# Kernel tuning notes

Measured on AMD Instinct MI355X. Metric: run time of the kernel, lower is better.

## Reference

```python
import jax, jax.numpy as jnp
import numpy as np

D_MODEL = 1024


def setup_inputs() -> dict:
    key = jax.random.key(0)
    ks = jax.random.split(key, 8)
    B, S, D = 32, 2048, D_MODEL
    scale = 1.0 / np.sqrt(D)
    return {
        "query": jax.random.normal(ks[0], (B, D), dtype=jnp.float32),
        "keys": jax.random.normal(ks[1], (B, S, D), dtype=jnp.float32),
        "Wq_w": jax.random.normal(ks[2], (D, D), dtype=jnp.float32) * scale,
        "Wq_b": jax.random.normal(ks[3], (D,), dtype=jnp.float32) * 0.01,
        "Wk_w": jax.random.normal(ks[4], (D, D), dtype=jnp.float32) * scale,
        "Wk_b": jax.random.normal(ks[5], (D,), dtype=jnp.float32) * 0.01,
        "v_w": jax.random.normal(ks[6], (D,), dtype=jnp.float32) * scale,
        "v_b": jax.random.normal(ks[7], (1,), dtype=jnp.float32) * 0.01,
    }


def reference(query, keys, Wq_w, Wq_b, Wk_w, Wk_b, v_w, v_b):
    # q: [B, 1, D], k: [B, S, D]
    q = (query @ Wq_w.T + Wq_b)[:, None, :]
    k = keys @ Wk_w.T + Wk_b
    # additive (Bahdanau) scores: [B, S]
    scores = jnp.einsum("bsd,d->bs", jnp.tanh(q + k), v_w) + v_b[0]
    attn = jax.nn.softmax(scores, axis=-1)
    # weighted sum over original keys: [B, D]
    context = jnp.einsum("bs,bsd->bd", attn, keys)
    return (context, attn)
```

## Files before the change

### kernel.cpp

```cpp
#include <hip/hip_runtime.h>
#include <cstddef>
#include <cstdint>

#define BATCH 32
#define SEQ 2048
#define DM 1024

typedef __attribute__((ext_vector_type(8))) _Float16 half8v;
typedef __attribute__((ext_vector_type(4))) _Float16 half4v;
typedef __attribute__((ext_vector_type(2))) __fp16 fp16x2;
typedef __attribute__((ext_vector_type(4))) float f32x4;

__device__ _Float16 g_Bpk[8 * 8 * 32 * 4 * 16 * 8];
__device__ float g_q[BATCH * DM];
__device__ float g_sp[16][BATCH * SEQ];

__device__ __forceinline__ float tanh_fast(float x) {
    float e = __expf(2.0f * x);
    return 1.0f - 2.0f / (e + 1.0f);
}

__global__ __launch_bounds__(256) void packb_kernel(const float* __restrict__ Wk_w) {
    int blk = blockIdx.x;
    int nc = blk >> 3, sub = blk & 7;
    int t = threadIdx.x;
    int row = t & 15, kgrp = (t >> 4) & 3, kt0 = t >> 6;
    const float* src = Wk_w + (size_t)(nc * 128 + sub * 16 + row) * DM;
    _Float16* dst = g_Bpk + (size_t)blk * 16384;
#pragma unroll
    for (int pass = 0; pass < 8; ++pass) {
        int kt = pass * 4 + kt0;
        float4 w0 = *reinterpret_cast<const float4*>(src + kt * 32 + kgrp * 8);
        float4 w1 = *reinterpret_cast<const float4*>(src + kt * 32 + kgrp * 8 + 4);
        union { _Float16 f[8]; half8v v; } h;
        h.f[0] = (_Float16)w0.x; h.f[1] = (_Float16)w0.y;
        h.f[2] = (_Float16)w0.z; h.f[3] = (_Float16)w0.w;
        h.f[4] = (_Float16)w1.x; h.f[5] = (_Float16)w1.y;
        h.f[6] = (_Float16)w1.z; h.f[7] = (_Float16)w1.w;
        *reinterpret_cast<half8v*>(&dst[(size_t)((kt * 4 + kgrp) * 16 + row) * 8]) = h.v;
    }
}

__global__ __launch_bounds__(256) void init_kernel(float* __restrict__ context) {
    int idx = blockIdx.x * 256 + threadIdx.x;
    if (idx < BATCH * DM) context[idx] = 0.f;
}

__global__ __launch_bounds__(256) void qproj_kernel(const float* __restrict__ query,
                                                    const float* __restrict__ Wq_w,
                                                    const float* __restrict__ Wq_b) {
    int d = blockIdx.x;
    int t = threadIdx.x;
    __shared__ float wrow[DM];
    __shared__ float part[8][32];
    reinterpret_cast<float4*>(wrow)[t] =
        reinterpret_cast<const float4*>(Wq_w + (size_t)d * DM)[t];
    __syncthreads();
    int b = t & 31, seg = t >> 5;
    const float4* qp = reinterpret_cast<const float4*>(query + b * DM + seg * 128);
    const float4* wp = reinterpret_cast<const float4*>(wrow + seg * 128);
    float acc = 0.f;
#pragma unroll
    for (int i = 0; i < 32; ++i) {
        float4 qv = qp[i];
        float4 wv = wp[i];
        acc += qv.x * wv.x + qv.y * wv.y + qv.z * wv.z + qv.w * wv.w;
    }
    part[seg][b] = acc;
    __syncthreads();
    if (t < 32) {
        float s = Wq_b[d];
#pragma unroll
        for (int g = 0; g < 8; ++g) s += part[g][t];
        g_q[t * DM + d] = s;
    }
}

#define BM 128
#define BN 128
#define NT2 16

__global__ __launch_bounds__(256, 3) void scores_kernel(const float* __restrict__ keys,
                                                        const float* __restrict__ Wk_b,
                                                        const float* __restrict__ v_w) {
    __shared__ _Float16 AhS[2][2][4][BM + 1][8];

    const unsigned bid = blockIdx.x;
    const unsigned L = (bid & 7u) * 512u + (bid >> 3);
    const int mtile = (int)(L >> 3);
    const int nchunk = (int)(L & 7u);
    const int m0 = mtile * BM;
    const int n0 = nchunk * BN;
    const int b = m0 >> 11;

    const int t = threadIdx.x;
    const int w = t >> 6, l = t & 63;
    const int wm = w >> 1, wn = w & 1;
    const int lr = l & 15, lg = l >> 4;

    const int akc = (l & 7) >> 1;
    const int aoff = ((l & 7) & 1) * 4;
    const float* Ap = keys + (size_t)(m0 + w * 32 + (l >> 3)) * DM + (l & 7) * 4;

    const _Float16* Bp = g_Bpk + ((size_t)(nchunk * 8 + wn * 4)) * 16384
                               + (size_t)(l >> 4) * 128 + (size_t)(l & 15) * 8;

    float4 as0[4], as1[4];
    half8v bE[4], bO[4];

    f32x4 acc[4][4];
#pragma unroll
    for (int mi = 0; mi < 4; ++mi)
#pragma unroll
        for (int ni = 0; ni < 4; ++ni)
#pragma unroll
            for (int c = 0; c < 4; ++c) acc[mi][ni][c] = 0.f;

#define LOAD_A2(kt)                                                              \
    {                                                                            \
        _Pragma("unroll") for (int j = 0; j < 4; ++j)                            \
            as0[j] = *reinterpret_cast<const float4*>(                           \
                Ap + (size_t)j * 8 * DM + (kt) * 64);                            \
        _Pragma("unroll") for (int j = 0; j < 4; ++j)                            \
            as1[j] = *reinterpret_cast<const float4*>(                           \
                Ap + (size_t)j * 8 * DM + (kt) * 64 + 32);                       \
    }
#define LOAD_BF(ks, dst)                                                         \
    {                                                                            \
        _Pragma("unroll") for (int ni = 0; ni < 4; ++ni)                         \
            dst[ni] = *reinterpret_cast<const half8v*>(                          \
                Bp + (size_t)ni * 16384 + (size_t)(ks) * 512);                   \
    }
#define STAGE_ONE(bufi, sub, areg)                                               \
    {                                                                            \
        _Pragma("unroll") for (int j = 0; j < 4; ++j) {                          \
            const float* fa = reinterpret_cast<const float*>(&areg[j]);          \
            union { fp16x2 h2[2]; half4v v; } u;                                 \
            u.h2[0] = __builtin_amdgcn_cvt_pkrtz(fa[0], fa[1]);                  \
            u.h2[1] = __builtin_amdgcn_cvt_pkrtz(fa[2], fa[3]);                  \
            *reinterpret_cast<half4v*>(                                          \
                &AhS[bufi][sub][akc][w * 32 + j * 8 + (l >> 3)][aoff]) = u.v;    \
        }                                                                        \
    }
#define COMPUTE_S(bufi, sub, breg)                                               \
    {                                                                            \
        __builtin_amdgcn_s_setprio(1);                                           \
        _Pragma("unroll") for (int mi = 0; mi < 4; ++mi) {                       \
            half8v ahv = *reinterpret_cast<const half8v*>(                       \
                &AhS[bufi][sub][lg][wm * 64 + mi * 16 + lr][0]);                 \
            _Pragma("unroll") for (int ni = 0; ni < 4; ++ni)                     \
                acc[mi][ni] = __builtin_amdgcn_mfma_f32_16x16x32_f16(            \
                    ahv, breg[ni], acc[mi][ni], 0, 0, 0);                        \
        }                                                                        \
        __builtin_amdgcn_s_setprio(0);                                          \
    }
#define SYNC()                                                                   \
    asm volatile("s_waitcnt lgkmcnt(0)" ::: "memory");                           \
    __builtin_amdgcn_s_barrier();                                                \
    asm volatile("" ::: "memory");

    LOAD_A2(0);
    LOAD_BF(0, bE);
    STAGE_ONE(0, 0, as0);
    STAGE_ONE(0, 1, as1);
    SYNC()

    for (int tt = 0; tt < NT2; ++tt) {
        const int cb = tt & 1;
        LOAD_BF(2 * tt + 1, bO);
        if (tt + 1 < NT2) LOAD_A2(tt + 1);
        COMPUTE_S(cb, 0, bE);
        COMPUTE_S(cb, 1, bO);
        if (tt + 1 < NT2) {
            STAGE_ONE(cb ^ 1, 0, as0);
            STAGE_ONE(cb ^ 1, 1, as1);
            LOAD_BF(2 * tt + 2, bE);
        }
        SYNC()
    }

    float qb[4], vw[4];
#pragma unroll
    for (int ni = 0; ni < 4; ++ni) {
        int n = n0 + wn * 64 + ni * 16 + lr;
        qb[ni] = g_q[b * DM + n] + Wk_b[n];
        vw[ni] = v_w[n];
    }
#pragma unroll
    for (int mi = 0; mi < 4; ++mi) {
#pragma unroll
        for (int rg = 0; rg < 4; ++rg) {
            float p = 0.f;
#pragma unroll
            for (int ni = 0; ni < 4; ++ni) {
                float val = acc[mi][ni][rg] + qb[ni];
                p += tanh_fast(val) * vw[ni];
            }
#pragma unroll
            for (int off = 8; off >= 1; off >>= 1) p += __shfl_xor(p, off, 16);
            if (lr == 0)
                g_sp[nchunk * 2 + wn][m0 + wm * 64 + mi * 16 + lg * 4 + rg] = p;
        }
    }
#undef LOAD_A2
#undef LOAD_BF
#undef STAGE_ONE
#undef COMPUTE_S
#undef SYNC
}

__global__ __launch_bounds__(256) void softmax_kernel(float* __restrict__ attn) {
    int b = blockIdx.x;
    int tid = threadIdx.x;
    __shared__ float redm[4];
    __shared__ float reds[4];
    float v[8];
    float mx = -1e30f;
#pragma unroll
    for (int i = 0; i < 8; ++i) {
        int idx = b * SEQ + i * 256 + tid;
        float s = 0.f;
#pragma unroll
        for (int pslot = 0; pslot < 16; ++pslot) s += g_sp[pslot][idx];
        v[i] = s;
        mx = fmaxf(mx, v[i]);
    }
#pragma unroll
    for (int off = 32; off >= 1; off >>= 1) mx = fmaxf(mx, __shfl_xor(mx, off));
    int wid = tid >> 6;
    if ((tid & 63) == 0) redm[wid] = mx;
    __syncthreads();
    mx = fmaxf(fmaxf(redm[0], redm[1]), fmaxf(redm[2], redm[3]));
    float sum = 0.f;
#pragma unroll
    for (int i = 0; i < 8; ++i) {
        v[i] = expf(v[i] - mx);
        sum += v[i];
    }
#pragma unroll
    for (int off = 32; off >= 1; off >>= 1) sum += __shfl_xor(sum, off);
    if ((tid & 63) == 0) reds[wid] = sum;
    __syncthreads();
    sum = reds[0] + reds[1] + reds[2] + reds[3];
    float inv = 1.f / sum;
#pragma unroll
    for (int i = 0; i < 8; ++i) attn[b * SEQ + i * 256 + tid] = v[i] * inv;
}

__global__ __launch_bounds__(256) void context_kernel(const float* __restrict__ keys,
                                                      const float* __restrict__ attn,
                                                      float* __restrict__ context) {
    int id = blockIdx.x;
    int schunk = id & 15;
    int b = id >> 4;
    int tid = threadIdx.x;
    __shared__ float a_s[128];
    if (tid < 128) a_s[tid] = attn[b * SEQ + schunk * 128 + tid];
    __syncthreads();
    const float4* kp =
        reinterpret_cast<const float4*>(keys + ((size_t)b * SEQ + schunk * 128) * DM) + tid;
    float4 acc = {0.f, 0.f, 0.f, 0.f};
#pragma unroll 4
    for (int s = 0; s < 128; ++s) {
        float4 kv = kp[(size_t)s * (DM / 4)];
        float a = a_s[s];
        acc.x += a * kv.x; acc.y += a * kv.y; acc.z += a * kv.z; acc.w += a * kv.w;
    }
    atomicAdd(&context[b * DM + tid * 4 + 0], acc.x);
    atomicAdd(&context[b * DM + tid * 4 + 1], acc.y);
    atomicAdd(&context[b * DM + tid * 4 + 2], acc.z);
    atomicAdd(&context[b * DM + tid * 4 + 3], acc.w);
}

extern "C" void kernel_launch(void* const* d_in, const int* in_sizes, int n_in,
                              void* d_out, int out_size, void* d_ws, size_t ws_size,
                              hipStream_t stream) {
    const float* query = (const float*)d_in[0];
    const float* keys  = (const float*)d_in[1];
    const float* Wq_w  = (const float*)d_in[2];
    const float* Wq_b  = (const float*)d_in[3];
    const float* Wk_w  = (const float*)d_in[4];
    const float* Wk_b  = (const float*)d_in[5];
    const float* v_w   = (const float*)d_in[6];

    float* context = (float*)d_out;
    float* attn    = context + BATCH * DM;

    hipLaunchKernelGGL(packb_kernel, dim3(64), dim3(256), 0, stream, Wk_w);
    hipLaunchKernelGGL(init_kernel, dim3(128), dim3(256), 0, stream, context);
    hipLaunchKernelGGL(qproj_kernel, dim3(DM), dim3(256), 0, stream, query, Wq_w, Wq_b);
    hipLaunchKernelGGL(scores_kernel, dim3((BATCH * SEQ / BM) * (DM / BN)), dim3(256), 0, stream,
                       keys, Wk_b, v_w);
    hipLaunchKernelGGL(softmax_kernel, dim3(BATCH), dim3(256), 0, stream, attn);
    hipLaunchKernelGGL(context_kernel, dim3(512), dim3(256), 0, stream, keys, attn, context);
}
```

Before: 255.7 us.

## Prepack keys to fp16 and stream A tiles via direct global-to-LDS loads

```diff
diff --git a/kernel.cpp b/kernel.cpp
--- a/kernel.cpp
+++ b/kernel.cpp
@@ -11,6 +11,7 @@
 typedef __attribute__((ext_vector_type(2))) __fp16 fp16x2;
 typedef __attribute__((ext_vector_type(4))) float f32x4;
 
+__device__ _Float16 g_Apk[(size_t)512 * 16 * 16 * 64 * 8];
 __device__ _Float16 g_Bpk[8 * 8 * 32 * 4 * 16 * 8];
 __device__ float g_q[BATCH * DM];
 __device__ float g_sp[16][BATCH * SEQ];
@@ -18,6 +19,33 @@
 __device__ __forceinline__ float tanh_fast(float x) {
     float e = __expf(2.0f * x);
     return 1.0f - 2.0f / (e + 1.0f);
+}
+
+__device__ __forceinline__ void gload16(const void* g, void* l) {
+    __builtin_amdgcn_global_load_lds((__attribute__((address_space(1))) void*)g,
+                                     (__attribute__((address_space(3))) void*)l, 16, 0, 0);
+}
+
+__global__ __launch_bounds__(256) void packa_kernel(const float* __restrict__ keys) {
+    int blk = blockIdx.x;
+    int mtile = blk >> 4, kt = blk & 15;
+    int t = threadIdx.x;
+    int row = t >> 1, half = t & 1;
+    int rh = row >> 6, r6 = row & 63;
+    const float* src = keys + (size_t)(mtile * 128 + row) * DM + kt * 64 + half * 32;
+    _Float16* dst = g_Apk + (size_t)blk * 8192;
+#pragma unroll
+    for (int kc = 0; kc < 4; ++kc) {
+        float4 w0 = *reinterpret_cast<const float4*>(src + kc * 8);
+        float4 w1 = *reinterpret_cast<const float4*>(src + kc * 8 + 4);
+        union { fp16x2 h2[4]; half8v v; } u;
+        u.h2[0] = __builtin_amdgcn_cvt_pkrtz(w0.x, w0.y);
+        u.h2[1] = __builtin_amdgcn_cvt_pkrtz(w0.z, w0.w);
+        u.h2[2] = __builtin_amdgcn_cvt_pkrtz(w1.x, w1.y);
+        u.h2[3] = __builtin_amdgcn_cvt_pkrtz(w1.z, w1.w);
+        int seg = (half * 4 + kc) * 2 + rh;
+        *reinterpret_cast<half8v*>(dst + (size_t)seg * 512 + r6 * 8) = u.v;
+    }
 }
 
 __global__ __launch_bounds__(256) void packb_kernel(const float* __restrict__ Wk_w) {
@@ -80,10 +108,9 @@
 #define BN 128
 #define NT2 16
 
-__global__ __launch_bounds__(256, 3) void scores_kernel(const float* __restrict__ keys,
-                                                        const float* __restrict__ Wk_b,
+__global__ __launch_bounds__(256, 4) void scores_kernel(const float* __restrict__ Wk_b,
                                                         const float* __restrict__ v_w) {
-    __shared__ _Float16 AhS[2][2][4][BM + 1][8];
+    __shared__ _Float16 AhS[2][16 * 520];
 
     const unsigned bid = blockIdx.x;
     const unsigned L = (bid & 7u) * 512u + (bid >> 3);
@@ -98,14 +125,11 @@
     const int wm = w >> 1, wn = w & 1;
     const int lr = l & 15, lg = l >> 4;
 
-    const int akc = (l & 7) >> 1;
-    const int aoff = ((l & 7) & 1) * 4;
-    const float* Ap = keys + (size_t)(m0 + w * 32 + (l >> 3)) * DM + (l & 7) * 4;
+    const int abase = (lg * 2 + wm) * 520 + lr * 8;
 
     const _Float16* Bp = g_Bpk + ((size_t)(nchunk * 8 + wn * 4)) * 16384
                                + (size_t)(l >> 4) * 128 + (size_t)(l & 15) * 8;
 
-    float4 as0[4], as1[4];
     half8v bE[4], bO[4];
 
     f32x4 acc[4][4];
@@ -116,14 +140,12 @@
 #pragma unroll
             for (int c = 0; c < 4; ++c) acc[mi][ni][c] = 0.f;
 
-#define LOAD_A2(kt)                                                              \
+#define ISSUE_A(kt, bufi)                                                        \
     {                                                                            \
-        _Pragma("unroll") for (int j = 0; j < 4; ++j)                            \
-            as0[j] = *reinterpret_cast<const float4*>(                           \
-                Ap + (size_t)j * 8 * DM + (kt) * 64);                            \
-        _Pragma("unroll") for (int j = 0; j < 4; ++j)                            \
-            as1[j] = *reinterpret_cast<const float4*>(                           \
-                Ap + (size_t)j * 8 * DM + (kt) * 64 + 32);                       \
+        const _Float16* ga = g_Apk + ((size_t)(mtile * 16 + (kt))) * 8192        \
+                           + (size_t)(w * 4) * 512 + (size_t)l * 8;              \
+        _Pragma("unroll") for (int i = 0; i < 4; ++i)                            \
+            gload16(ga + i * 512, &AhS[bufi][(w * 4 + i) * 520]);                \
     }
 #define LOAD_BF(ks, dst)                                                         \
     {                                                                            \
@@ -131,52 +153,35 @@
             dst[ni] = *reinterpret_cast<const half8v*>(                          \
                 Bp + (size_t)ni * 16384 + (size_t)(ks) * 512);                   \
     }
-#define STAGE_ONE(bufi, sub, areg)                                               \
-    {                                                                            \
-        _Pragma("unroll") for (int j = 0; j < 4; ++j) {                          \
-            const float* fa = reinterpret_cast<const float*>(&areg[j]);          \
-            union { fp16x2 h2[2]; half4v v; } u;                                 \
-            u.h2[0] = __builtin_amdgcn_cvt_pkrtz(fa[0], fa[1]);                  \
-            u.h2[1] = __builtin_amdgcn_cvt_pkrtz(fa[2], fa[3]);                  \
-            *reinterpret_cast<half4v*>(                                          \
-                &AhS[bufi][sub][akc][w * 32 + j * 8 + (l >> 3)][aoff]) = u.v;    \
-        }                                                                        \
-    }
 #define COMPUTE_S(bufi, sub, breg)                                               \
     {                                                                            \
         __builtin_amdgcn_s_setprio(1);                                           \
         _Pragma("unroll") for (int mi = 0; mi < 4; ++mi) {                       \
             half8v ahv = *reinterpret_cast<const half8v*>(                       \
-                &AhS[bufi][sub][lg][wm * 64 + mi * 16 + lr][0]);                 \
+                &AhS[bufi][abase + (sub) * 4160 + mi * 128]);                    \
             _Pragma("unroll") for (int ni = 0; ni < 4; ++ni)                     \
                 acc[mi][ni] = __builtin_amdgcn_mfma_f32_16x16x32_f16(            \
                     ahv, breg[ni], acc[mi][ni], 0, 0, 0);                        \
         }                                                                        \
         __builtin_amdgcn_s_setprio(0);                                          \
     }
-#define SYNC()                                                                   \
-    asm volatile("s_waitcnt lgkmcnt(0)" ::: "memory");                           \
-    __builtin_amdgcn_s_barrier();                                                \
+
+    ISSUE_A(0, 0);
+    LOAD_BF(0, bE);
+    asm volatile("s_waitcnt vmcnt(0)" ::: "memory");
+    __builtin_amdgcn_s_barrier();
     asm volatile("" ::: "memory");
-
-    LOAD_A2(0);
-    LOAD_BF(0, bE);
-    STAGE_ONE(0, 0, as0);
-    STAGE_ONE(0, 1, as1);
-    SYNC()
 
     for (int tt = 0; tt < NT2; ++tt) {
         const int cb = tt & 1;
+        if (tt + 1 < NT2) ISSUE_A(tt + 1, cb ^ 1);
         LOAD_BF(2 * tt + 1, bO);
-        if (tt + 1 < NT2) LOAD_A2(tt + 1);
         COMPUTE_S(cb, 0, bE);
         COMPUTE_S(cb, 1, bO);
-        if (tt + 1 < NT2) {
-            STAGE_ONE(cb ^ 1, 0, as0);
-            STAGE_ONE(cb ^ 1, 1, as1);
-            LOAD_BF(2 * tt + 2, bE);
-        }
-        SYNC()
+        if (tt + 1 < NT2) LOAD_BF(2 * tt + 2, bE);
+        asm volatile("s_waitcnt vmcnt(4)" ::: "memory");
+        __builtin_amdgcn_s_barrier();
+        asm volatile("" ::: "memory");
     }
 
     float qb[4], vw[4];
@@ -202,11 +207,9 @@
                 g_sp[nchunk * 2 + wn][m0 + wm * 64 + mi * 16 + lg * 4 + rg] = p;
         }
     }
-#undef LOAD_A2
+#undef ISSUE_A
 #undef LOAD_BF
-#undef STAGE_ONE
 #undef COMPUTE_S
-#undef SYNC
 }
 
 __global__ __launch_bounds__(256) void softmax_kernel(float* __restrict__ attn) {
@@ -286,11 +289,12 @@
     float* context = (float*)d_out;
     float* attn    = context + BATCH * DM;
 
+    hipLaunchKernelGGL(packa_kernel, dim3(8192), dim3(256), 0, stream, keys);
     hipLaunchKernelGGL(packb_kernel, dim3(64), dim3(256), 0, stream, Wk_w);
     hipLaunchKernelGGL(init_kernel, dim3(128), dim3(256), 0, stream, context);
     hipLaunchKernelGGL(qproj_kernel, dim3(DM), dim3(256), 0, stream, query, Wq_w, Wq_b);
     hipLaunchKernelGGL(scores_kernel, dim3((BATCH * SEQ / BM) * (DM / BN)), dim3(256), 0, stream,
-                       keys, Wk_b, v_w);
+                       Wk_b, v_w);
     hipLaunchKernelGGL(softmax_kernel, dim3(BATCH), dim3(256), 0, stream, attn);
     hipLaunchKernelGGL(context_kernel, dim3(512), dim3(256), 0, stream, keys, attn, context);
 }
```

After: 310.0 us. 21.2% more time.
